# Kernel tuning notes

Hardware: AMD Instinct MI355X
Metric: run time of the kernel (lower is better)

## Reference

```python
import jax, jax.numpy as jnp
import numpy as np

X_SIZE, NUM_NEURONS, Z_SIZE = 2048, 4096, 64
D = X_SIZE + NUM_NEURONS + Z_SIZE  # 6208
TOPK, ZTOPK = 16, 8
EPS_TIE = 1e-9
RND = 0.5  # stand-in for random.random(); tie indicator t is 0 w.p. 1 for continuous inputs


def setup_inputs() -> dict:
    key = jax.random.key(0)
    k1, k2, k3, k4, k5 = jax.random.split(key, 5)
    x = jax.random.normal(k1, (X_SIZE,), dtype=jnp.float32)
    z = jax.random.normal(k2, (Z_SIZE,), dtype=jnp.float32)
    y_response = jax.random.uniform(k3, (NUM_NEURONS,), dtype=jnp.float32)
    neurons = jax.random.normal(k4, (D, D), dtype=jnp.float32)
    ages = 1.0 + 9.0 * jax.random.uniform(k5, (D,), dtype=jnp.float32)  # ages >= 1
    return {"x": x, "z": z, "y_response": y_response, "neurons": neurons, "ages": ages}


def _update_rows(neurons, ages, inpt, idx, vals):
    # Faithful to update_neuron_weights, including the (1,k)@(k,D) row-mix
    # that broadcasts the same mixed row to all k winner rows.
    a = ages[idx]                                   # (k,)
    upd = (vals / a)[:, None] * inpt[None, :]       # (k, D)
    mix = jnp.einsum('k,kd->d', (a - 1.0) / a, neurons[idx])  # (D,)
    new_rows = mix[None, :] + upd                   # (k, D)
    norm = jnp.sqrt(jnp.sum(new_rows * new_rows, axis=1, keepdims=True)) + 1e-12
    neurons = neurons.at[idx].set(new_rows / norm)
    ages = ages.at[idx].add(1.0)
    return neurons, ages


def reference(x, z, y_response, neurons, ages):
    # Steady-state path: num_neurons_init == max_num_neurons (> topk),
    # supervized_z = supervized_x = None, xtopk = None.
    x0, x1 = 0, X_SIZE
    y0, y1 = X_SIZE, X_SIZE + NUM_NEURONS
    z0 = X_SIZE + NUM_NEURONS

    inpt = jnp.concatenate([x, y_response, z])      # (D,)
    response = neurons @ inpt                       # (D,)
    final = jnp.zeros_like(response)

    # --- z path: top-(ztopk) winners, normalized against runner-up ---
    zvals, zidx = jax.lax.top_k(response[z0:], ZTOPK + 1)
    gz = z0 + zidx
    final = final.at[gz[:-1]].set((zvals[:-1] - zvals[-1]) / (zvals[0] - zvals[-1]))
    neurons, ages = _update_rows(neurons, ages, inpt, gz[:-1], zvals[:-1])

    # --- x path (xtopk None, unsupervised): normalize full x response ---
    rx = response[x0:x1]
    tx = jnp.where(jnp.all(rx == 0.0), 1.0, 0.0)
    xvals = rx / (jnp.max(rx) + EPS_TIE * tx * RND)
    final = final.at[x0:x1].set(xvals)
    xidx = jnp.arange(x0, x1)
    neurons, ages = _update_rows(neurons, ages, inpt, xidx[:-1], xvals[:-1])

    # --- y path: fully grown net -> topk winner-take-most branch ---
    yvals, yidx = jax.lax.top_k(response[y0:y1], TOPK + 1)
    gy = y0 + yidx
    ty = jnp.where(jnp.any(yvals[:-1] == yvals[-1]), 1.0, 0.0)
    final = final.at[gy[:-1]].set(
        (yvals[:-1] - yvals[-1]) / (yvals[0] - yvals[-1] + EPS_TIE * ty * RND))
    neurons, ages = _update_rows(neurons, ages, inpt, gy[:-1], yvals[:-1])

    z_response = final[z0:]
    return z_response, final, neurons, ages
```

## Files before the change

### kernel.cpp

```cpp
#include <hip/hip_runtime.h>
#include <math.h>

typedef float v4f __attribute__((ext_vector_type(4)));

#define XS 2048
#define NN 4096
#define ZS 64
#define DD 6208
#define D4 1552
#define Z0 (XS + NN)
#define TOPK 16
#define ZTOPK 8
#define EPS_TIE 1e-9f
#define RNDC 0.5f
#define NXUPD 2047

#define OUT_FINAL 64
#define OUT_NEUR  (64 + DD)
#define OUT_AGES  (OUT_NEUR + (size_t)DD * DD)

#define WS_RESP   0
#define WS_INPT   DD
#define WS_MIXX   (2 * DD)
#define WS_MIXZ   (3 * DD)
#define WS_MIXY   (4 * DD)
#define WS_SCAL   (5 * DD)
#define WS_SELROW (WS_SCAL + 32)
#define WS_SELC   (WS_SELROW + 24)
#define WS_SELW   (WS_SELC + 24)
#define WS_TOTAL  (WS_SELW + 32)

#define XBLKS 1024
#define CSPL  388

__device__ __forceinline__ v4f ld4(const float* p) { return *(const v4f*)p; }
__device__ __forceinline__ v4f v4z() { v4f v; v.x = v.y = v.z = v.w = 0.f; return v; }
__device__ __forceinline__ float dot4(v4f a, v4f b) {
  return fmaf(a.x, b.x, fmaf(a.y, b.y, fmaf(a.z, b.z, a.w * b.w)));
}
__device__ __forceinline__ v4f load_inpt(const float* x, const float* yr,
                                         const float* zv, int c) {
  int col = c * 4;
  if (col < XS) return ld4(x + col);
  if (col < Z0) return ld4(yr + (col - XS));
  return ld4(zv + (col - Z0));
}

__global__ __launch_bounds__(256) void k_phase1(
    const float* __restrict__ x, const float* __restrict__ yr,
    const float* __restrict__ zv, const float* __restrict__ neurons,
    const float* __restrict__ ages, float* __restrict__ ws,
    float* __restrict__ outn)
{
  const int t = threadIdx.x;
  const int b = blockIdx.x;

  if (b < XBLKS) {
    const int rg = b >> 2, cs = b & 3;
    const int row0 = rg * 8;
    const int cbase = cs * CSPL;
    const int c0 = cbase + t;
    const int c1 = cbase + 256 + t;
    const bool has1 = (t < CSPL - 256);

    v4f i0 = load_inpt(x, yr, zv, c0);
    v4f i1 = has1 ? load_inpt(x, yr, zv, c1) : v4z();
    if (b < 4) {
      ((v4f*)(ws + WS_INPT))[c0] = i0;
      if (has1) ((v4f*)(ws + WS_INPT))[c1] = i1;
    }

    float wr[8];
    #pragma unroll
    for (int r = 0; r < 8; ++r) {
      float a = ages[row0 + r];
      wr[r] = (row0 + r < NXUPD) ? (a - 1.f) / a : 0.f;
    }

    float dot[8];
    v4f m0 = v4z(), m1 = v4z();
    #pragma unroll
    for (int r = 0; r < 8; ++r) {
      const int row = row0 + r;
      const float* rp = neurons + (size_t)row * DD;
      v4f a0 = ld4(rp + 4 * c0);
      v4f a1 = has1 ? ld4(rp + 4 * c1) : v4z();
      dot[r] = dot4(a0, i0) + dot4(a1, i1);
      m0 += wr[r] * a0;
      m1 += wr[r] * a1;
      if (row >= NXUPD) {
        __builtin_nontemporal_store(a0, (v4f*)(outn + (size_t)row * DD + 4 * c0));
        if (has1)
          __builtin_nontemporal_store(a1, (v4f*)(outn + (size_t)row * DD + 4 * c1));
      }
    }

    __shared__ float wred[4][8];
    const int lane = t & 63, wv = t >> 6;
    #pragma unroll
    for (int r = 0; r < 8; ++r) {
      float v = dot[r];
      #pragma unroll
      for (int m = 32; m >= 1; m >>= 1) v += __shfl_xor(v, m);
      if (lane == 0) wred[wv][r] = v;
    }
    __syncthreads();
    if (t < 8)
      atomicAdd(ws + WS_RESP + row0 + t,
                wred[0][t] + wred[1][t] + wred[2][t] + wred[3][t]);

    atomicAdd(ws + WS_MIXX + 4 * c0 + 0, m0.x);
    atomicAdd(ws + WS_MIXX + 4 * c0 + 1, m0.y);
    atomicAdd(ws + WS_MIXX + 4 * c0 + 2, m0.z);
    atomicAdd(ws + WS_MIXX + 4 * c0 + 3, m0.w);
    if (has1) {
      atomicAdd(ws + WS_MIXX + 4 * c1 + 0, m1.x);
      atomicAdd(ws + WS_MIXX + 4 * c1 + 1, m1.y);
      atomicAdd(ws + WS_MIXX + 4 * c1 + 2, m1.z);
      atomicAdd(ws + WS_MIXX + 4 * c1 + 3, m1.w);
    }
  } else {
    const int row = 2048 + (b - XBLKS);
    const float* rp = neurons + (size_t)row * DD;
    float* op = outn + (size_t)row * DD;
    float dot = 0.f;
    #pragma unroll
    for (int k = 0; k < 6; ++k) {
      const int c = t + 256 * k;
      v4f a = ld4(rp + 4 * c);
      v4f iv = load_inpt(x, yr, zv, c);
      dot += dot4(a, iv);
      __builtin_nontemporal_store(a, (v4f*)(op + 4 * c));
    }
    if (t < 16) {
      const int c = 1536 + t;
      v4f a = ld4(rp + 4 * c);
      v4f iv = ld4(zv + (4 * c - Z0));
      dot += dot4(a, iv);
      __builtin_nontemporal_store(a, (v4f*)(op + 4 * c));
    }
    __shared__ float red[4];
    const int lane = t & 63, wv = t >> 6;
    #pragma unroll
    for (int m = 32; m >= 1; m >>= 1) dot += __shfl_xor(dot, m);
    if (lane == 0) red[wv] = dot;
    __syncthreads();
    if (t == 0) ws[WS_RESP + row] = red[0] + red[1] + red[2] + red[3];
  }
}

__global__ __launch_bounds__(1024) void k_phase2(
    const float* __restrict__ ages, float* __restrict__ ws, float* __restrict__ out)
{
  const int t = threadIdx.x;
  __shared__ float sv[NN];
  __shared__ float swv[64];
  __shared__ int   swi[16];
  __shared__ float s_zval[ZTOPK + 1];
  __shared__ int   s_zidx[ZTOPK + 1];
  __shared__ float s_yval[TOPK + 1];
  __shared__ int   s_yidx[TOPK + 1];
  __shared__ float s_denx, s_ty;
  __shared__ float s_z64[ZS];

  float* resp = ws + WS_RESP;

  if (t < ZS) s_z64[t] = resp[Z0 + t];
  __syncthreads();
  if (t < 64) {
    float v = s_z64[t];
    for (int j = 0; j <= ZTOPK; ++j) {
      float bv = v; int bi = t;
      #pragma unroll
      for (int m = 1; m < 64; m <<= 1) {
        float ov = __shfl_xor(bv, m);
        int   oi = __shfl_xor(bi, m);
        if (ov > bv || (ov == bv && oi < bi)) { bv = ov; bi = oi; }
      }
      if (t == 0) { s_zval[j] = bv; s_zidx[j] = bi; }
      if (t == bi) v = -INFINITY;
    }
  }

  float lm = -INFINITY; int nz = 0;
  for (int i = t; i < XS; i += 1024) { float v = resp[i]; lm = fmaxf(lm, v); nz |= (v != 0.f); }
  #pragma unroll
  for (int m = 1; m < 64; m <<= 1) { lm = fmaxf(lm, __shfl_xor(lm, m)); nz |= __shfl_xor(nz, m); }
  if ((t & 63) == 0) { swv[t >> 6] = lm; swi[t >> 6] = nz; }
  __syncthreads();
  if (t == 0) {
    float m2 = -INFINITY; int n2 = 0;
    for (int q = 0; q < 16; ++q) { m2 = fmaxf(m2, swv[q]); n2 |= swi[q]; }
    float tx = n2 ? 0.f : 1.f;
    s_denx = m2 + EPS_TIE * tx * RNDC;
  }
  __syncthreads();

  for (int i = t; i < NN; i += 1024) sv[i] = resp[XS + i];
  __syncthreads();
  for (int j = 0; j <= TOPK; ++j) {
    float bv = -INFINITY; int bi = 0x7fffffff;
    for (int i = t; i < NN; i += 1024) { float v = sv[i]; if (v > bv || (v == bv && i < bi)) { bv = v; bi = i; } }
    #pragma unroll
    for (int m = 1; m < 64; m <<= 1) {
      float ov = __shfl_xor(bv, m); int oi = __shfl_xor(bi, m);
      if (ov > bv || (ov == bv && oi < bi)) { bv = ov; bi = oi; }
    }
    if ((t & 63) == 0) { swv[t >> 6] = bv; swi[t >> 6] = bi; }
    __syncthreads();
    if (t == 0) {
      float b2 = -INFINITY; int i2 = 0x7fffffff;
      for (int q = 0; q < 16; ++q)
        if (swv[q] > b2 || (swv[q] == b2 && swi[q] < i2)) { b2 = swv[q]; i2 = swi[q]; }
      s_yval[j] = b2; s_yidx[j] = i2; sv[i2] = -INFINITY;
    }
    __syncthreads();
  }
  if (t == 0) {
    float ty = 0.f;
    for (int q = 0; q < TOPK; ++q) if (s_yval[q] == s_yval[TOPK]) ty = 1.f;
    s_ty = ty;
  }
  __syncthreads();

  const float denx  = s_denx;
  const float zlast = s_zval[ZTOPK];
  const float zden  = s_zval[0] - zlast;
  const float ylast = s_yval[TOPK];
  const float yden  = s_yval[0] - ylast + EPS_TIE * s_ty * RNDC;
  float* fin = out + OUT_FINAL;
  for (int i = t; i < DD; i += 1024) {
    float v = 0.f;
    if (i < XS) v = resp[i] / denx;
    fin[i] = v;
  }
  __syncthreads();
  if (t < ZTOPK)                  fin[Z0 + s_zidx[t]] = (s_zval[t] - zlast) / zden;
  else if (t >= 32 && t < 32 + TOPK) { int k = t - 32; fin[XS + s_yidx[k]] = (s_yval[k] - ylast) / yden; }
  if (t >= 128 && t < 192) {
    int i = t - 128;
    float v = 0.f;
    for (int k = 0; k < ZTOPK; ++k) if (s_zidx[k] == i) v = (s_zval[k] - zlast) / zden;
    out[i] = v;
  }

  float* oag = out + OUT_AGES;
  for (int i = t; i < DD; i += 1024) oag[i] = ages[i] + ((i < NXUPD) ? 1.f : 0.f);
  __syncthreads();
  if (t < ZTOPK + TOPK) {
    int row = (t < ZTOPK) ? (Z0 + s_zidx[t]) : (XS + s_yidx[t - ZTOPK]);
    oag[row] = ages[row] + 1.f;
  }

  float sii = 0.f, smm = 0.f, smi = 0.f;
  float* inpt = ws + WS_INPT;
  float* mixx = ws + WS_MIXX;
  for (int i = t; i < DD; i += 1024) {
    float ip = inpt[i], mx = mixx[i];
    sii = fmaf(ip, ip, sii); smm = fmaf(mx, mx, smm); smi = fmaf(mx, ip, smi);
  }
  #pragma unroll
  for (int m = 1; m < 64; m <<= 1) {
    sii += __shfl_xor(sii, m); smm += __shfl_xor(smm, m); smi += __shfl_xor(smi, m);
  }
  __syncthreads();
  if ((t & 63) == 0) { int w = t >> 6; swv[w] = sii; swv[16 + w] = smm; swv[32 + w] = smi; }
  __syncthreads();
  if (t == 0) {
    float a = 0.f, b = 0.f, c = 0.f;
    for (int q = 0; q < 16; ++q) { a += swv[q]; b += swv[16 + q]; c += swv[32 + q]; }
    float* scal = ws + WS_SCAL;
    scal[0] = a; scal[1] = b; scal[2] = c; scal[7] = denx;
  }

  if (t < ZTOPK) {
    int row = Z0 + s_zidx[t];
    ((int*)(ws + WS_SELROW))[t] = row;
    float a = ages[row];
    ws[WS_SELC + t] = s_zval[t] / a;
    ws[WS_SELW + t] = (a - 1.f) / a;
  } else if (t >= 32 && t < 32 + TOPK) {
    int k = t - 32;
    int row = XS + s_yidx[k];
    ((int*)(ws + WS_SELROW))[ZTOPK + k] = row;
    float a = ages[row];
    ws[WS_SELC + ZTOPK + k] = s_yval[k] / a;
    ws[WS_SELW + ZTOPK + k] = (a - 1.f) / a;
  }
}

__global__ __launch_bounds__(256) void k_phase3a(
    const float* __restrict__ neurons, float* __restrict__ ws)
{
  const int b = blockIdx.x;
  const int t = threadIdx.x;
  const int row = ((const int*)(ws + WS_SELROW))[b];
  const float w = ws[WS_SELW + b];
  float* dst = ws + ((b < ZTOPK) ? WS_MIXZ : WS_MIXY);
  const float* src = neurons + (size_t)row * DD;
  #pragma unroll
  for (int k = 0; k < 6; ++k) {
    const int c = t + 256 * k;
    v4f a = ld4(src + 4 * c);
    atomicAdd(dst + 4 * c + 0, w * a.x);
    atomicAdd(dst + 4 * c + 1, w * a.y);
    atomicAdd(dst + 4 * c + 2, w * a.z);
    atomicAdd(dst + 4 * c + 3, w * a.w);
  }
  if (t < 16) {
    const int c = 1536 + t;
    v4f a = ld4(src + 4 * c);
    atomicAdd(dst + 4 * c + 0, w * a.x);
    atomicAdd(dst + 4 * c + 1, w * a.y);
    atomicAdd(dst + 4 * c + 2, w * a.z);
    atomicAdd(dst + 4 * c + 3, w * a.w);
  }
}

__global__ __launch_bounds__(1024) void k_phase3b(float* __restrict__ ws)
{
  const int t = threadIdx.x;
  __shared__ float red[64];
  float* inpt = ws + WS_INPT;
  float smmz = 0.f, smiz = 0.f, smmy = 0.f, smiy = 0.f;
  for (int i = t; i < DD; i += 1024) {
    float ip = inpt[i];
    float mz = ws[WS_MIXZ + i], my = ws[WS_MIXY + i];
    smmz = fmaf(mz, mz, smmz); smiz = fmaf(mz, ip, smiz);
    smmy = fmaf(my, my, smmy); smiy = fmaf(my, ip, smiy);
  }
  #pragma unroll
  for (int m = 1; m < 64; m <<= 1) {
    smmz += __shfl_xor(smmz, m); smiz += __shfl_xor(smiz, m);
    smmy += __shfl_xor(smmy, m); smiy += __shfl_xor(smiy, m);
  }
  __syncthreads();
  if ((t & 63) == 0) { int w = t >> 6; red[w] = smmz; red[16 + w] = smiz; red[32 + w] = smmy; red[48 + w] = smiy; }
  __syncthreads();
  if (t == 0) {
    float a = 0.f, b = 0.f, c = 0.f, d = 0.f;
    for (int q = 0; q < 16; ++q) { a += red[q]; b += red[16 + q]; c += red[32 + q]; d += red[48 + q]; }
    ws[WS_SCAL + 3] = a; ws[WS_SCAL + 4] = b; ws[WS_SCAL + 5] = c; ws[WS_SCAL + 6] = d;
  }
}

__global__ __launch_bounds__(256) void k_phase4(
    const float* __restrict__ ages, const float* __restrict__ ws,
    float* __restrict__ outn)
{
  const int b = blockIdx.x;
  const int t = threadIdx.x;
  const float sii = ws[WS_SCAL + 0];
  int row; float c, smm, smi; const float* mix;
  if (b < NXUPD) {
    row = b;
    float a = ages[row];
    c = (ws[WS_RESP + row] / ws[WS_SCAL + 7]) / a;
    mix = ws + WS_MIXX; smm = ws[WS_SCAL + 1]; smi = ws[WS_SCAL + 2];
  } else {
    int k = b - NXUPD;
    row = ((const int*)(ws + WS_SELROW))[k];
    c = ws[WS_SELC + k];
    if (k < ZTOPK) { mix = ws + WS_MIXZ; smm = ws[WS_SCAL + 3]; smi = ws[WS_SCAL + 4]; }
    else           { mix = ws + WS_MIXY; smm = ws[WS_SCAL + 5]; smi = ws[WS_SCAL + 6]; }
  }
  const float inv = 1.f / (sqrtf(fmaf(c, fmaf(c, sii, 2.f * smi), smm)) + 1e-12f);
  const float* inpt = ws + WS_INPT;
  float* dst = outn + (size_t)row * DD;
  #pragma unroll
  for (int k = 0; k < 6; ++k) {
    const int i = t + 256 * k;
    v4f m4 = ((const v4f*)(mix))[i];
    v4f i4 = ((const v4f*)(inpt))[i];
    v4f o = (m4 + c * i4) * inv;
    __builtin_nontemporal_store(o, (v4f*)dst + i);
  }
  if (t < 16) {
    const int i = 1536 + t;
    v4f m4 = ((const v4f*)(mix))[i];
    v4f i4 = ((const v4f*)(inpt))[i];
    v4f o = (m4 + c * i4) * inv;
    __builtin_nontemporal_store(o, (v4f*)dst + i);
  }
}

extern "C" void kernel_launch(void* const* d_in, const int* in_sizes, int n_in,
                              void* d_out, int out_size, void* d_ws, size_t ws_size,
                              hipStream_t stream)
{
  (void)in_sizes; (void)n_in; (void)out_size; (void)ws_size;
  const float* x    = (const float*)d_in[0];
  const float* zin  = (const float*)d_in[1];
  const float* yr   = (const float*)d_in[2];
  const float* neur = (const float*)d_in[3];
  const float* ages = (const float*)d_in[4];
  float* out = (float*)d_out;
  float* ws  = (float*)d_ws;

  hipMemsetAsync(d_ws, 0, (size_t)WS_TOTAL * sizeof(float), stream);
  k_phase1<<<XBLKS + (DD - XS), 256, 0, stream>>>(x, yr, zin, neur, ages, ws, out + OUT_NEUR);
  k_phase2<<<1, 1024, 0, stream>>>(ages, ws, out);
  k_phase3a<<<ZTOPK + TOPK, 256, 0, stream>>>(neur, ws);
  k_phase3b<<<1, 1024, 0, stream>>>(ws);
  k_phase4<<<NXUPD + ZTOPK + TOPK, 256, 0, stream>>>(ages, ws, out + OUT_NEUR);
}
```

Measured before the change: 360.7 us.

## Restructure phase1 into full-row blocks with replicated mix scratch and faster top-k

Phase1 now gives each x-block eight full rows with the input held in registers. Its x-mix accumulation goes to eight replicated scratch rows inside the output buffer instead of one contended workspace array, which cuts the atomic contention and removes the response atomics. The y/z blocks each handle two rows. Row 2047's pass-through copy moves into the x-blocks, and nontemporal stores become plain stores. Phase2's y top-k becomes a two-level per-wave candidate selection with fewer block barriers. Phase3a writes scaled rows to scratch that phase3b sums across 16 blocks instead of using atomics. The change relies on output rows being overwritten later, adds an extra memset and scratch traffic, and has fewer blocks on the x rows.

```diff
diff --git a/kernel.cpp b/kernel.cpp
--- a/kernel.cpp
+++ b/kernel.cpp
@@ -19,6 +19,7 @@
 #define OUT_NEUR  (64 + DD)
 #define OUT_AGES  (OUT_NEUR + (size_t)DD * DD)
 
+
 #define WS_RESP   0
 #define WS_INPT   DD
 #define WS_MIXX   (2 * DD)
@@ -30,10 +31,11 @@
 #define WS_SELW   (WS_SELC + 24)
 #define WS_TOTAL  (WS_SELW + 32)
 
-#define XBLKS 1024
-#define CSPL  388
+#define XBLKS 256
+#define YZBLKS 2080
 
 __device__ __forceinline__ v4f ld4(const float* p) { return *(const v4f*)p; }
+__device__ __forceinline__ void st4(float* p, v4f v) { *(v4f*)p = v; }
 __device__ __forceinline__ v4f v4z() { v4f v; v.x = v.y = v.z = v.w = 0.f; return v; }
 __device__ __forceinline__ float dot4(v4f a, v4f b) {
   return fmaf(a.x, b.x, fmaf(a.y, b.y, fmaf(a.z, b.z, a.w * b.w)));
@@ -55,105 +57,132 @@
   const int t = threadIdx.x;
   const int b = blockIdx.x;
 
+  v4f iv[6];
+  #pragma unroll
+  for (int k = 0; k < 6; ++k) iv[k] = load_inpt(x, yr, zv, t + 256 * k);
+  v4f ive = v4z();
+  if (t < 16) ive = ld4(zv + 4 * t + (4 * 1536 - Z0));
+
+  if (b == 0) {
+    #pragma unroll
+    for (int k = 0; k < 6; ++k) ((v4f*)(ws + WS_INPT))[t + 256 * k] = iv[k];
+    if (t < 16) ((v4f*)(ws + WS_INPT))[1536 + t] = ive;
+  }
+
   if (b < XBLKS) {
-    const int rg = b >> 2, cs = b & 3;
-    const int row0 = rg * 8;
-    const int cbase = cs * CSPL;
-    const int c0 = cbase + t;
-    const int c1 = cbase + 256 + t;
-    const bool has1 = (t < CSPL - 256);
-
-    v4f i0 = load_inpt(x, yr, zv, c0);
-    v4f i1 = has1 ? load_inpt(x, yr, zv, c1) : v4z();
-    if (b < 4) {
-      ((v4f*)(ws + WS_INPT))[c0] = i0;
-      if (has1) ((v4f*)(ws + WS_INPT))[c1] = i1;
-    }
-
-    float wr[8];
-    #pragma unroll
-    for (int r = 0; r < 8; ++r) {
-      float a = ages[row0 + r];
-      wr[r] = (row0 + r < NXUPD) ? (a - 1.f) / a : 0.f;
-    }
-
-    float dot[8];
-    v4f m0 = v4z(), m1 = v4z();
+    const int row0 = b * 8;
+    v4f macc[6];
+    #pragma unroll
+    for (int k = 0; k < 6; ++k) macc[k] = v4z();
+    v4f mace = v4z();
+    float dots[8];
+
     #pragma unroll
     for (int r = 0; r < 8; ++r) {
       const int row = row0 + r;
       const float* rp = neurons + (size_t)row * DD;
-      v4f a0 = ld4(rp + 4 * c0);
-      v4f a1 = has1 ? ld4(rp + 4 * c1) : v4z();
-      dot[r] = dot4(a0, i0) + dot4(a1, i1);
-      m0 += wr[r] * a0;
-      m1 += wr[r] * a1;
-      if (row >= NXUPD) {
-        __builtin_nontemporal_store(a0, (v4f*)(outn + (size_t)row * DD + 4 * c0));
-        if (has1)
-          __builtin_nontemporal_store(a1, (v4f*)(outn + (size_t)row * DD + 4 * c1));
+      const float age = ages[row];
+      const float w = (row < NXUPD) ? (age - 1.f) / age : 0.f;
+      v4f av[6];
+      #pragma unroll
+      for (int k = 0; k < 6; ++k) av[k] = ld4(rp + 4 * (t + 256 * k));
+      v4f ae = v4z();
+      if (t < 16) ae = ld4(rp + 4 * (1536 + t));
+      float d = 0.f;
+      #pragma unroll
+      for (int k = 0; k < 6; ++k) {
+        d += dot4(av[k], iv[k]);
+        macc[k] += w * av[k];
       }
+      d += dot4(ae, ive);
+      mace += w * ae;
+      if (row == 2047) {
+        float* op = outn + (size_t)row * DD;
+        #pragma unroll
+        for (int k = 0; k < 6; ++k) st4(op + 4 * (t + 256 * k), av[k]);
+        if (t < 16) st4(op + 4 * (1536 + t), ae);
+      }
+      dots[r] = d;
     }
 
     __shared__ float wred[4][8];
     const int lane = t & 63, wv = t >> 6;
     #pragma unroll
     for (int r = 0; r < 8; ++r) {
-      float v = dot[r];
+      float v = dots[r];
       #pragma unroll
       for (int m = 32; m >= 1; m >>= 1) v += __shfl_xor(v, m);
       if (lane == 0) wred[wv][r] = v;
     }
     __syncthreads();
     if (t < 8)
-      atomicAdd(ws + WS_RESP + row0 + t,
-                wred[0][t] + wred[1][t] + wred[2][t] + wred[3][t]);
-
-    atomicAdd(ws + WS_MIXX + 4 * c0 + 0, m0.x);
-    atomicAdd(ws + WS_MIXX + 4 * c0 + 1, m0.y);
-    atomicAdd(ws + WS_MIXX + 4 * c0 + 2, m0.z);
-    atomicAdd(ws + WS_MIXX + 4 * c0 + 3, m0.w);
-    if (has1) {
-      atomicAdd(ws + WS_MIXX + 4 * c1 + 0, m1.x);
-      atomicAdd(ws + WS_MIXX + 4 * c1 + 1, m1.y);
-      atomicAdd(ws + WS_MIXX + 4 * c1 + 2, m1.z);
-      atomicAdd(ws + WS_MIXX + 4 * c1 + 3, m1.w);
-    }
-  } else {
-    const int row = 2048 + (b - XBLKS);
-    const float* rp = neurons + (size_t)row * DD;
-    float* op = outn + (size_t)row * DD;
-    float dot = 0.f;
+      ws[WS_RESP + row0 + t] = wred[0][t] + wred[1][t] + wred[2][t] + wred[3][t];
+
+    float* mrep = outn + (size_t)(24 + (b & 7)) * DD;
     #pragma unroll
     for (int k = 0; k < 6; ++k) {
       const int c = t + 256 * k;
-      v4f a = ld4(rp + 4 * c);
-      v4f iv = load_inpt(x, yr, zv, c);
-      dot += dot4(a, iv);
-      __builtin_nontemporal_store(a, (v4f*)(op + 4 * c));
+      atomicAdd(mrep + 4 * c + 0, macc[k].x);
+      atomicAdd(mrep + 4 * c + 1, macc[k].y);
+      atomicAdd(mrep + 4 * c + 2, macc[k].z);
+      atomicAdd(mrep + 4 * c + 3, macc[k].w);
     }
     if (t < 16) {
       const int c = 1536 + t;
-      v4f a = ld4(rp + 4 * c);
-      v4f iv = ld4(zv + (4 * c - Z0));
-      dot += dot4(a, iv);
-      __builtin_nontemporal_store(a, (v4f*)(op + 4 * c));
-    }
-    __shared__ float red[4];
+      atomicAdd(mrep + 4 * c + 0, mace.x);
+      atomicAdd(mrep + 4 * c + 1, mace.y);
+      atomicAdd(mrep + 4 * c + 2, mace.z);
+      atomicAdd(mrep + 4 * c + 3, mace.w);
+    }
+  } else {
+    const int row0 = 2048 + 2 * (b - XBLKS);
+    const float* rp0 = neurons + (size_t)row0 * DD;
+    const float* rp1 = rp0 + DD;
+    float* op0 = outn + (size_t)row0 * DD;
+    float* op1 = op0 + DD;
+
+    v4f a0[6], a1[6];
+    #pragma unroll
+    for (int k = 0; k < 6; ++k) a0[k] = ld4(rp0 + 4 * (t + 256 * k));
+    #pragma unroll
+    for (int k = 0; k < 6; ++k) a1[k] = ld4(rp1 + 4 * (t + 256 * k));
+    v4f ae0 = v4z(), ae1 = v4z();
+    if (t < 16) { ae0 = ld4(rp0 + 4 * (1536 + t)); ae1 = ld4(rp1 + 4 * (1536 + t)); }
+
+    float d0 = 0.f, d1 = 0.f;
+    #pragma unroll
+    for (int k = 0; k < 6; ++k) {
+      d0 += dot4(a0[k], iv[k]);
+      st4(op0 + 4 * (t + 256 * k), a0[k]);
+    }
+    #pragma unroll
+    for (int k = 0; k < 6; ++k) {
+      d1 += dot4(a1[k], iv[k]);
+      st4(op1 + 4 * (t + 256 * k), a1[k]);
+    }
+    if (t < 16) {
+      d0 += dot4(ae0, ive); d1 += dot4(ae1, ive);
+      st4(op0 + 4 * (1536 + t), ae0);
+      st4(op1 + 4 * (1536 + t), ae1);
+    }
+
+    __shared__ float red[4][2];
     const int lane = t & 63, wv = t >> 6;
     #pragma unroll
-    for (int m = 32; m >= 1; m >>= 1) dot += __shfl_xor(dot, m);
-    if (lane == 0) red[wv] = dot;
+    for (int m = 32; m >= 1; m >>= 1) { d0 += __shfl_xor(d0, m); d1 += __shfl_xor(d1, m); }
+    if (lane == 0) { red[wv][0] = d0; red[wv][1] = d1; }
     __syncthreads();
-    if (t == 0) ws[WS_RESP + row] = red[0] + red[1] + red[2] + red[3];
+    if (t < 2)
+      ws[WS_RESP + row0 + t] = red[0][t] + red[1][t] + red[2][t] + red[3][t];
   }
 }
 
 __global__ __launch_bounds__(1024) void k_phase2(
-    const float* __restrict__ ages, float* __restrict__ ws, float* __restrict__ out)
+    const float* __restrict__ ages, float* __restrict__ ws,
+    float* __restrict__ out, const float* __restrict__ outn)
 {
   const int t = threadIdx.x;
-  __shared__ float sv[NN];
+  const int wv = t >> 6, lane = t & 63;
   __shared__ float swv[64];
   __shared__ int   swi[16];
   __shared__ float s_zval[ZTOPK + 1];
@@ -162,6 +191,8 @@
   __shared__ int   s_yidx[TOPK + 1];
   __shared__ float s_denx, s_ty;
   __shared__ float s_z64[ZS];
+  __shared__ float s_cv[272];
+  __shared__ int   s_ci[272];
 
   float* resp = ws + WS_RESP;
 
@@ -186,7 +217,7 @@
   for (int i = t; i < XS; i += 1024) { float v = resp[i]; lm = fmaxf(lm, v); nz |= (v != 0.f); }
   #pragma unroll
   for (int m = 1; m < 64; m <<= 1) { lm = fmaxf(lm, __shfl_xor(lm, m)); nz |= __shfl_xor(nz, m); }
-  if ((t & 63) == 0) { swv[t >> 6] = lm; swi[t >> 6] = nz; }
+  if (lane == 0) { swv[wv] = lm; swi[wv] = nz; }
   __syncthreads();
   if (t == 0) {
     float m2 = -INFINITY; int n2 = 0;
@@ -194,28 +225,53 @@
     float tx = n2 ? 0.f : 1.f;
     s_denx = m2 + EPS_TIE * tx * RNDC;
   }
-  __syncthreads();
-
-  for (int i = t; i < NN; i += 1024) sv[i] = resp[XS + i];
-  __syncthreads();
-  for (int j = 0; j <= TOPK; ++j) {
-    float bv = -INFINITY; int bi = 0x7fffffff;
-    for (int i = t; i < NN; i += 1024) { float v = sv[i]; if (v > bv || (v == bv && i < bi)) { bv = v; bi = i; } }
+
+  float yvv[4]; int yii[4];
+  #pragma unroll
+  for (int j = 0; j < 4; ++j) {
+    int idx = wv * 256 + j * 64 + lane;
+    yvv[j] = resp[XS + idx];
+    yii[j] = idx;
+  }
+  for (int p = 0; p <= TOPK; ++p) {
+    float bv = yvv[0]; int bi = yii[0];
+    #pragma unroll
+    for (int j = 1; j < 4; ++j)
+      if (yvv[j] > bv || (yvv[j] == bv && yii[j] < bi)) { bv = yvv[j]; bi = yii[j]; }
     #pragma unroll
     for (int m = 1; m < 64; m <<= 1) {
       float ov = __shfl_xor(bv, m); int oi = __shfl_xor(bi, m);
       if (ov > bv || (ov == bv && oi < bi)) { bv = ov; bi = oi; }
     }
-    if ((t & 63) == 0) { swv[t >> 6] = bv; swi[t >> 6] = bi; }
-    __syncthreads();
-    if (t == 0) {
-      float b2 = -INFINITY; int i2 = 0x7fffffff;
-      for (int q = 0; q < 16; ++q)
-        if (swv[q] > b2 || (swv[q] == b2 && swi[q] < i2)) { b2 = swv[q]; i2 = swi[q]; }
-      s_yval[j] = b2; s_yidx[j] = i2; sv[i2] = -INFINITY;
-    }
-    __syncthreads();
-  }
+    if (lane == 0) { s_cv[wv * 17 + p] = bv; s_ci[wv * 17 + p] = bi; }
+    #pragma unroll
+    for (int j = 0; j < 4; ++j) if (yii[j] == bi) yvv[j] = -INFINITY;
+  }
+  __syncthreads();
+  if (wv == 0) {
+    float mv[5]; int mi[5];
+    #pragma unroll
+    for (int q = 0; q < 5; ++q) {
+      int e = q * 64 + lane;
+      if (e < 272) { mv[q] = s_cv[e]; mi[q] = s_ci[e]; }
+      else         { mv[q] = -INFINITY; mi[q] = 0x7fffffff; }
+    }
+    for (int p = 0; p <= TOPK; ++p) {
+      float bv = mv[0]; int bi = mi[0];
+      #pragma unroll
+      for (int q = 1; q < 5; ++q)
+        if (mv[q] > bv || (mv[q] == bv && mi[q] < bi)) { bv = mv[q]; bi = mi[q]; }
+      #pragma unroll
+      for (int m = 1; m < 64; m <<= 1) {
+        float ov = __shfl_xor(bv, m); int oi = __shfl_xor(bi, m);
+        if (ov > bv || (ov == bv && oi < bi)) { bv = ov; bi = oi; }
+      }
+      if (lane == 0) { s_yval[p] = bv; s_yidx[p] = bi; }
+      #pragma unroll
+      for (int q = 0; q < 5; ++q) if (mi[q] == bi) mv[q] = -INFINITY;
+    }
+  }
+  __syncthreads();
   if (t == 0) {
     float ty = 0.f;
     for (int q = 0; q < TOPK; ++q) if (s_yval[q] == s_yval[TOPK]) ty = 1.f;
@@ -252,6 +308,17 @@
     oag[row] = ages[row] + 1.f;
   }
 
+  {
+    const float* mrep = outn + 24 * (size_t)DD;
+    for (int i = t; i < DD; i += 1024) {
+      float s = 0.f;
+      #pragma unroll
+      for (int r = 0; r < 8; ++r) s += mrep[(size_t)r * DD + i];
+      ws[WS_MIXX + i] = s;
+    }
+  }
+  __syncthreads();
+
   float sii = 0.f, smm = 0.f, smi = 0.f;
   float* inpt = ws + WS_INPT;
   float* mixx = ws + WS_MIXX;
@@ -264,7 +331,7 @@
     sii += __shfl_xor(sii, m); smm += __shfl_xor(smm, m); smi += __shfl_xor(smi, m);
   }
   __syncthreads();
-  if ((t & 63) == 0) { int w = t >> 6; swv[w] = sii; swv[16 + w] = smm; swv[32 + w] = smi; }
+  if (lane == 0) { swv[wv] = sii; swv[16 + wv] = smm; swv[32 + wv] = smi; }
   __syncthreads();
   if (t == 0) {
     float a = 0.f, b = 0.f, c = 0.f;
@@ -290,57 +357,55 @@
 }
 
 __global__ __launch_bounds__(256) void k_phase3a(
-    const float* __restrict__ neurons, float* __restrict__ ws)
+    const float* __restrict__ neurons, const float* __restrict__ ws,
+    float* __restrict__ outn)
 {
   const int b = blockIdx.x;
   const int t = threadIdx.x;
   const int row = ((const int*)(ws + WS_SELROW))[b];
   const float w = ws[WS_SELW + b];
-  float* dst = ws + ((b < ZTOPK) ? WS_MIXZ : WS_MIXY);
   const float* src = neurons + (size_t)row * DD;
+  float* dst = outn + (size_t)b * DD;
   #pragma unroll
   for (int k = 0; k < 6; ++k) {
     const int c = t + 256 * k;
-    v4f a = ld4(src + 4 * c);
-    atomicAdd(dst + 4 * c + 0, w * a.x);
-    atomicAdd(dst + 4 * c + 1, w * a.y);
-    atomicAdd(dst + 4 * c + 2, w * a.z);
-    atomicAdd(dst + 4 * c + 3, w * a.w);
+    st4(dst + 4 * c, w * ld4(src + 4 * c));
   }
   if (t < 16) {
     const int c = 1536 + t;
-    v4f a = ld4(src + 4 * c);
-    atomicAdd(dst + 4 * c + 0, w * a.x);
-    atomicAdd(dst + 4 * c + 1, w * a.y);
-    atomicAdd(dst + 4 * c + 2, w * a.z);
-    atomicAdd(dst + 4 * c + 3, w * a.w);
-  }
-}
-
-__global__ __launch_bounds__(1024) void k_phase3b(float* __restrict__ ws)
+    st4(dst + 4 * c, w * ld4(src + 4 * c));
+  }
+}
+
+__global__ __launch_bounds__(256) void k_phase3b(
+    const float* __restrict__ outn, float* __restrict__ ws)
 {
   const int t = threadIdx.x;
-  __shared__ float red[64];
-  float* inpt = ws + WS_INPT;
   float smmz = 0.f, smiz = 0.f, smmy = 0.f, smiy = 0.f;
-  for (int i = t; i < DD; i += 1024) {
-    float ip = inpt[i];
-    float mz = ws[WS_MIXZ + i], my = ws[WS_MIXY + i];
-    smmz = fmaf(mz, mz, smmz); smiz = fmaf(mz, ip, smiz);
-    smmy = fmaf(my, my, smmy); smiy = fmaf(my, ip, smiy);
-  }
-  #pragma unroll
-  for (int m = 1; m < 64; m <<= 1) {
+  for (int i = blockIdx.x * 256 + t; i < DD; i += 16 * 256) {
+    float ip = ws[WS_INPT + i];
+    float sz = 0.f, sy = 0.f;
+    #pragma unroll
+    for (int r = 0; r < 8; ++r)  sz += outn[(size_t)r * DD + i];
+    #pragma unroll
+    for (int r = 8; r < 24; ++r) sy += outn[(size_t)r * DD + i];
+    ws[WS_MIXZ + i] = sz;
+    ws[WS_MIXY + i] = sy;
+    smmz = fmaf(sz, sz, smmz); smiz = fmaf(sz, ip, smiz);
+    smmy = fmaf(sy, sy, smmy); smiy = fmaf(sy, ip, smiy);
+  }
+  __shared__ float red[4][4];
+  const int lane = t & 63, wv = t >> 6;
+  #pragma unroll
+  for (int m = 32; m >= 1; m >>= 1) {
     smmz += __shfl_xor(smmz, m); smiz += __shfl_xor(smiz, m);
     smmy += __shfl_xor(smmy, m); smiy += __shfl_xor(smiy, m);
   }
-  __syncthreads();
-  if ((t & 63) == 0) { int w = t >> 6; red[w] = smmz; red[16 + w] = smiz; red[32 + w] = smmy; red[48 + w] = smiy; }
-  __syncthreads();
-  if (t == 0) {
-    float a = 0.f, b = 0.f, c = 0.f, d = 0.f;
-    for (int q = 0; q < 16; ++q) { a += red[q]; b += red[16 + q]; c += red[32 + q]; d += red[48 + q]; }
-    ws[WS_SCAL + 3] = a; ws[WS_SCAL + 4] = b; ws[WS_SCAL + 5] = c; ws[WS_SCAL + 6] = d;
+  if (lane == 0) { red[wv][0] = smmz; red[wv][1] = smiz; red[wv][2] = smmy; red[wv][3] = smiy; }
+  __syncthreads();
+  if (t < 4) {
+    float s = red[0][t] + red[1][t] + red[2][t] + red[3][t];
+    atomicAdd(ws + WS_SCAL + 3 + t, s);
   }
 }
 
@@ -370,17 +435,13 @@
   #pragma unroll
   for (int k = 0; k < 6; ++k) {
     const int i = t + 256 * k;
-    v4f m4 = ((const v4f*)(mix))[i];
-    v4f i4 = ((const v4f*)(inpt))[i];
-    v4f o = (m4 + c * i4) * inv;
-    __builtin_nontemporal_store(o, (v4f*)dst + i);
+    v4f o = (((const v4f*)mix)[i] + c * ((const v4f*)inpt)[i]) * inv;
+    st4(dst + 4 * i, o);
   }
   if (t < 16) {
     const int i = 1536 + t;
-    v4f m4 = ((const v4f*)(mix))[i];
-    v4f i4 = ((const v4f*)(inpt))[i];
-    v4f o = (m4 + c * i4) * inv;
-    __builtin_nontemporal_store(o, (v4f*)dst + i);
+    v4f o = (((const v4f*)mix)[i] + c * ((const v4f*)inpt)[i]) * inv;
+    st4(dst + 4 * i, o);
   }
 }
 
@@ -396,11 +457,13 @@
   const float* ages = (const float*)d_in[4];
   float* out = (float*)d_out;
   float* ws  = (float*)d_ws;
+  float* outn = out + OUT_NEUR;
 
   hipMemsetAsync(d_ws, 0, (size_t)WS_TOTAL * sizeof(float), stream);
-  k_phase1<<<XBLKS + (DD - XS), 256, 0, stream>>>(x, yr, zin, neur, ages, ws, out + OUT_NEUR);
-  k_phase2<<<1, 1024, 0, stream>>>(ages, ws, out);
-  k_phase3a<<<ZTOPK + TOPK, 256, 0, stream>>>(neur, ws);
-  k_phase3b<<<1, 1024, 0, stream>>>(ws);
-  k_phase4<<<NXUPD + ZTOPK + TOPK, 256, 0, stream>>>(ages, ws, out + OUT_NEUR);
-}
+  hipMemsetAsync(outn + 24 * (size_t)DD, 0, 8 * (size_t)DD * sizeof(float), stream);
+  k_phase1<<<XBLKS + YZBLKS, 256, 0, stream>>>(x, yr, zin, neur, ages, ws, outn);
+  k_phase2<<<1, 1024, 0, stream>>>(ages, ws, out, outn);
+  k_phase3a<<<ZTOPK + TOPK, 256, 0, stream>>>(neur, ws, outn);
+  k_phase3b<<<16, 256, 0, stream>>>(outn, ws);
+  k_phase4<<<NXUPD + ZTOPK + TOPK, 256, 0, stream>>>(ages, ws, outn);
+}
```

Measured after the change: 361.8 us. About the same (+0.3%).
